# Kernel optimization log

Hardware: AMD Instinct MI355X
Metric: run time of the kernel (lower is better)

## Reference

```python
import jax, jax.numpy as jnp
import numpy as np

DIM = 1024
H = 16
D = DIM // H
CS = 64  # chunk_size
SCALE = D ** -0.5


def setup_inputs() -> dict:
    key = jax.random.key(0)
    k1, k2, k3 = jax.random.split(key, 3)
    B, N = 4, 4096
    x = jax.random.normal(k1, (B, N, DIM), dtype=jnp.float32)
    # torch nn.Linear(dim, 3*dim, bias=False): y = x @ W.T, W:[3*dim, dim].
    # We store the transposed layout W_qkv:[dim, 3*dim] so y = x @ W_qkv.
    W_qkv = jax.random.normal(k2, (DIM, 3 * DIM), dtype=jnp.float32) * (DIM ** -0.5)
    W_out = jax.random.normal(k3, (DIM, DIM), dtype=jnp.float32) * (DIM ** -0.5)
    return {"x": x, "W_qkv": W_qkv, "W_out": W_out}


def reference(x, W_qkv, W_out):
    B, N, C = x.shape
    qkv = (x @ W_qkv).reshape(B, N, 3, H, D)
    qkv = jnp.transpose(qkv, (2, 0, 3, 1, 4))  # [3,B,H,N,D]
    q, k, v = qkv[0], qkv[1], qkv[2]
    # N chosen divisible by CS, so no padding needed (pad=0 branch).
    nc = N // CS
    q = q.reshape(B, H, nc, CS, D)
    k = k.reshape(B, H, nc, CS, D)
    v = v.reshape(B, H, nc, CS, D)
    # Local quadratic attention within each chunk, causal mask.
    attn = jnp.einsum('bhcqd,bhckd->bhcqk', q, k) * SCALE
    mask = jnp.triu(jnp.ones((CS, CS), dtype=bool), k=1)
    attn = jnp.where(mask, jnp.float32(-65000.0), attn)
    attn = jax.nn.softmax(attn, axis=-1)
    out_local = jnp.einsum('bhcqk,bhckd->bhcqd', attn, v)
    # Cross-chunk linear term (num_chunks > 1): mean-pooled K/V, exclusive cumsum.
    chunk_k = k.mean(axis=3)  # [B,H,nc,D]
    chunk_v = v.mean(axis=3)
    cum_k = jnp.cumsum(chunk_k, axis=2)
    cum_v = jnp.cumsum(chunk_v, axis=2)
    zeros = jnp.zeros((B, H, 1, D), dtype=x.dtype)
    cum_k = jnp.concatenate([zeros, cum_k[:, :, :-1]], axis=2)
    cum_v = jnp.concatenate([zeros, cum_v[:, :, :-1]], axis=2)
    cross = jax.nn.sigmoid(jnp.einsum('bhcsd,bhcd->bhcs', q, cum_k) * SCALE)
    out = out_local + cross[..., None] * cum_v[:, :, :, None, :] * 0.5
    out = out.reshape(B, H, N, D)
    out = jnp.transpose(out, (0, 2, 1, 3)).reshape(B, N, C)
    return out @ W_out
```

## Files before the change

### kernel.cpp

```cpp
#include <hip/hip_runtime.h>
#include <stdint.h>

typedef __attribute__((ext_vector_type(4))) float f32x4;
typedef __attribute__((ext_vector_type(8))) short short8;
typedef unsigned short u16;

#define NH 16
#define HD 64
#define SEQ 4096
#define BATCH 4
#define NROWS (BATCH * SEQ)
#define DIMC 1024
#define QKVC 3072
#define SCALE 0.125f

__device__ __forceinline__ u16 f2bf(float f) {
  union { float f; uint32_t u; } v; v.f = f;
  uint32_t u = v.u;
  uint32_t r = (u + 0x7fffu + ((u >> 16) & 1u)) >> 16;
  return (u16)r;
}
__device__ __forceinline__ float bf2f(u16 h) {
  union { uint32_t u; float f; } v; v.u = ((uint32_t)h) << 16;
  return v.f;
}

__global__ __launch_bounds__(256) void cvt_kernel(const float* __restrict__ in,
                                                  u16* __restrict__ out, int n4) {
  int i = blockIdx.x * 256 + threadIdx.x;
  if (i >= n4) return;
  float4 v = ((const float4*)in)[i];
  ushort4 o;
  o.x = f2bf(v.x); o.y = f2bf(v.y); o.z = f2bf(v.z); o.w = f2bf(v.w);
  ((ushort4*)out)[i] = o;
}

__global__ __launch_bounds__(256) void transpose_cvt(const float* __restrict__ in,
                                                     u16* __restrict__ out, int R, int C) {
  __shared__ float t[32][33];
  int nbx = C >> 5;
  int bx = blockIdx.x % nbx, by = blockIdx.x / nbx;
  int r0 = by << 5, c0 = bx << 5;
  int tid = threadIdx.x;
#pragma unroll
  for (int i = 0; i < 4; i++) {
    int id = i * 256 + tid; int lr = id >> 5, lc = id & 31;
    t[lr][lc] = in[(size_t)(r0 + lr) * C + (c0 + lc)];
  }
  __syncthreads();
#pragma unroll
  for (int i = 0; i < 4; i++) {
    int id = i * 256 + tid; int lr = id >> 5, lc = id & 31;
    out[(size_t)(c0 + lr) * R + (r0 + lc)] = f2bf(t[lc][lr]);
  }
}

template <int OUT_BF16, int DO_SUMS>
__global__ __launch_bounds__(512, 2) void gemm_bt(const u16* __restrict__ A,
                                                  const u16* __restrict__ Bt,
                                                  void* __restrict__ Cv,
                                                  float* __restrict__ chk,
                                                  float* __restrict__ chv,
                                                  int M, int N, int K) {
  __shared__ __align__(16) u16 lds2[2][32768];
  int nbx = N >> 8;
  int nwg = gridDim.x;
  int bid = blockIdx.x;
  int cpx = nwg >> 3;
  int swz = (bid & 7) * cpx + (bid >> 3);
  int bx = swz % nbx, by = swz / nbx;
  int tid = threadIdx.x, lane = tid & 63, wv = tid >> 6;
  int wr = wv >> 2, wc = wv & 3;
  int lr = lane & 15, g = lane >> 4;
  int rx = lr & 7;
  int rsub = lane >> 3;
  int clog = (lane & 7) ^ rsub;

  const u16* Ap = A + (size_t)(by * 256) * K;
  const u16* Bp = Bt + (size_t)(bx * 256) * K;

  f32x4 acc[8][4];
#pragma unroll
  for (int m = 0; m < 8; m++)
#pragma unroll
    for (int n = 0; n < 4; n++) acc[m][n] = (f32x4){0.f, 0.f, 0.f, 0.f};

  short8 a0[4][2], a1[4][2], b0[2][2], b1[2][2];

#define ISSUE_A(HALF, L, T) do {                                                \
    int ru_ = (HALF) * 128 + (L) * 64 + wv * 8;                                 \
    const u16* g_ = Ap + (size_t)(ru_ + rsub) * K + (T) * 64 + clog * 8;        \
    __builtin_amdgcn_global_load_lds(                                           \
        (const __attribute__((address_space(1))) uint32_t*)g_,                  \
        (__attribute__((address_space(3))) uint32_t*)&lds2[(T) & 1][ru_ * 64],  \
        16, 0, 0);                                                              \
  } while (0)

#define ISSUE_B(HALF, L, T) do {                                                \
    int ru_ = (HALF) * 128 + (L) * 64 + wv * 8;                                 \
    const u16* g_ = Bp + (size_t)(ru_ + rsub) * K + (T) * 64 + clog * 8;        \
    __builtin_amdgcn_global_load_lds(                                           \
        (const __attribute__((address_space(1))) uint32_t*)g_,                  \
        (__attribute__((address_space(3)))                                      \
             uint32_t*)&lds2[(T) & 1][16384 + ru_ * 64],                        \
        16, 0, 0);                                                              \
  } while (0)

#define LDA4(DST, MH, T) do {                                                   \
    _Pragma("unroll")                                                           \
    for (int m2 = 0; m2 < 4; m2++) {                                            \
      int row_ = wr * 128 + ((MH) * 4 + m2) * 16 + lr;                          \
      const u16* bp_ = &lds2[(T) & 1][row_ * 64];                               \
      _Pragma("unroll")                                                         \
      for (int s = 0; s < 2; s++)                                               \
        DST[m2][s] = *(const short8*)(bp_ + (((s * 4 + g) ^ rx) << 3));         \
    }                                                                           \
  } while (0)

#define LDB(DST, NHh, T) do {                                                   \
    _Pragma("unroll")                                                           \
    for (int n2 = 0; n2 < 2; n2++) {                                            \
      int row_ = wc * 64 + ((NHh) * 2 + n2) * 16 + lr;                          \
      const u16* bp_ = &lds2[(T) & 1][16384 + row_ * 64];                       \
      _Pragma("unroll")                                                         \
      for (int s = 0; s < 2; s++)                                               \
        DST[n2][s] = *(const short8*)(bp_ + (((s * 4 + g) ^ rx) << 3));         \
    }                                                                           \
  } while (0)

#define MFMA_Q(MH, NHh, AA, BB) do {                                            \
    _Pragma("unroll")                                                           \
    for (int s = 0; s < 2; s++)                                                 \
      _Pragma("unroll")                                                         \
      for (int m2 = 0; m2 < 4; m2++)                                            \
        _Pragma("unroll")                                                       \
        for (int n2 = 0; n2 < 2; n2++)                                          \
          acc[(MH) * 4 + m2][(NHh) * 2 + n2] =                                  \
              __builtin_amdgcn_mfma_f32_16x16x32_bf16(                          \
                  AA[m2][s], BB[n2][s], acc[(MH) * 4 + m2][(NHh) * 2 + n2],     \
                  0, 0, 0);                                                     \
  } while (0)

  int NT = K >> 6;
  ISSUE_A(0, 0, 0); ISSUE_A(0, 1, 0); ISSUE_A(1, 0, 0); ISSUE_A(1, 1, 0);
  ISSUE_B(0, 0, 0); ISSUE_B(0, 1, 0); ISSUE_B(1, 0, 0); ISSUE_B(1, 1, 0);
  __syncthreads();

  for (int t = 0; t < NT; t++) {
    LDA4(a0, 0, t);
    LDB(b0, 0, t);
    __builtin_amdgcn_sched_barrier(0);
    if (t + 1 < NT) {
      ISSUE_A(0, 0, t + 1); ISSUE_A(0, 1, t + 1);
      ISSUE_A(1, 0, t + 1); ISSUE_A(1, 1, t + 1);
    }
    __builtin_amdgcn_sched_barrier(0);
    LDB(b1, 1, t);
    LDA4(a1, 1, t);
    __builtin_amdgcn_sched_barrier(0);
    if (t + 1 < NT) {
      ISSUE_B(0, 0, t + 1); ISSUE_B(0, 1, t + 1);
      ISSUE_B(1, 0, t + 1); ISSUE_B(1, 1, t + 1);
    }
    __builtin_amdgcn_sched_barrier(0);
    __builtin_amdgcn_s_setprio(1);
    MFMA_Q(0, 0, a0, b0);
    __builtin_amdgcn_sched_barrier(0);
    MFMA_Q(0, 1, a0, b1);
    __builtin_amdgcn_sched_barrier(0);
    MFMA_Q(1, 1, a1, b1);
    __builtin_amdgcn_sched_barrier(0);
    MFMA_Q(1, 0, a1, b0);
    __builtin_amdgcn_s_setprio(0);
    __syncthreads();
  }

#undef ISSUE_A
#undef ISSUE_B
#undef LDA4
#undef LDB
#undef MFMA_Q

  int rb = by * 256 + wr * 128, cb = bx * 256 + wc * 64;

  if (DO_SUMS && cb >= 1024) {
#pragma unroll
    for (int mh = 0; mh < 2; mh++)
#pragma unroll
      for (int n = 0; n < 4; n++) {
        float sum = 0.f;
#pragma unroll
        for (int m = mh * 4; m < mh * 4 + 4; m++)
#pragma unroll
          for (int r = 0; r < 4; r++) sum += acc[m][n][r];
        sum += __shfl_xor(sum, 16);
        sum += __shfl_xor(sum, 32);
        if (g == 0) {
          int grb = rb + mh * 64;
          int b = grb >> 12, c = (grb >> 6) & 63;
          int cg = cb + n * 16 + lr;
          int col = cg & 1023;
          int h = col >> 6, d = col & 63;
          float* dst = (cg < 2048) ? chk : chv;
          dst[(((size_t)(b * 16 + h)) * 64 + c) * 64 + d] = sum * 0.015625f;
        }
      }
  }

#pragma unroll
  for (int m = 0; m < 8; m++)
#pragma unroll
    for (int n = 0; n < 4; n++)
#pragma unroll
      for (int r = 0; r < 4; r++) {
        int rg = rb + m * 16 + g * 4 + r;
        int cg = cb + n * 16 + lr;
        float v = acc[m][n][r];
        if (OUT_BF16)
          ((u16*)Cv)[(size_t)rg * N + cg] = f2bf(v);
        else
          ((float*)Cv)[(size_t)rg * N + cg] = v;
      }
}

__global__ __launch_bounds__(256) void cumsum_excl(const float* __restrict__ ck,
                                                   const float* __restrict__ cv,
                                                   float* __restrict__ cuk,
                                                   float* __restrict__ cuv) {
  __shared__ float qk[4][64], qv[4][64];
  int bh = blockIdx.x;
  int d = threadIdx.x & 63, q = threadIdx.x >> 6;
  size_t base = ((size_t)bh * 64) * 64 + d;
  float sk = 0.f, sv = 0.f;
  for (int c = q * 16; c < q * 16 + 16; c++) {
    sk += ck[base + (size_t)c * 64];
    sv += cv[base + (size_t)c * 64];
  }
  qk[q][d] = sk; qv[q][d] = sv;
  __syncthreads();
  float ak = 0.f, av = 0.f;
  for (int p = 0; p < q; p++) { ak += qk[p][d]; av += qv[p][d]; }
  for (int c = q * 16; c < q * 16 + 16; c++) {
    size_t i = base + (size_t)c * 64;
    cuk[i] = ak; cuv[i] = av;
    ak += ck[i]; av += cv[i];
  }
}

__global__ __launch_bounds__(256) void attn_kernel(const u16* __restrict__ qkv,
                                                   const float* __restrict__ cuk,
                                                   const float* __restrict__ cuv,
                                                   u16* __restrict__ out) {
  int blk = blockIdx.x;
  int c = blk & 63, h = (blk >> 6) & 15, b = blk >> 10;
  int row0 = b * SEQ + c * 64;
  __shared__ u16 qp_s[64][88];
  __shared__ u16 k_s[64][88];
  __shared__ u16 vt_s[64][88];
  __shared__ u16 ck_s[64];
  __shared__ float cv_s[64];
  int tid = threadIdx.x;
  {
    if (tid < 64) {
      ck_s[tid] = f2bf(cuk[(size_t)blk * 64 + tid]);
      cv_s[tid] = cuv[(size_t)blk * 64 + tid];
    }
    int r = tid >> 2, qt = tid & 3;
    const u16* rp = qkv + (size_t)(row0 + r) * QKVC + h * 64 + qt * 16;
    uint4 q0 = *(const uint4*)rp;          uint4 q1 = *(const uint4*)(rp + 8);
    uint4 k0 = *(const uint4*)(rp + 1024); uint4 k1 = *(const uint4*)(rp + 1032);
    uint4 v0 = *(const uint4*)(rp + 2048); uint4 v1 = *(const uint4*)(rp + 2056);
    *(uint4*)&qp_s[r][qt * 16] = q0;    *(uint4*)&qp_s[r][qt * 16 + 8] = q1;
    *(uint4*)&k_s[r][qt * 16] = k0;     *(uint4*)&k_s[r][qt * 16 + 8] = k1;
    const u16* vv0 = (const u16*)&v0;   const u16* vv1 = (const u16*)&v1;
    int vcol = (r & 7) | ((((r >> 3) ^ qt) & 7) << 3);
#pragma unroll
    for (int j = 0; j < 8; j++) vt_s[qt * 16 + j][vcol] = vv0[j];
#pragma unroll
    for (int j = 0; j < 8; j++) vt_s[qt * 16 + 8 + j][vcol] = vv1[j];
  }
  __syncthreads();

  int lane = tid & 63, w = tid >> 6;
  int lr = lane & 15, g = lane >> 4;
  f32x4 accS[4];
#pragma unroll
  for (int n = 0; n < 4; n++) accS[n] = (f32x4){0.f, 0.f, 0.f, 0.f};
  f32x4 accC = (f32x4){0.f, 0.f, 0.f, 0.f};
  short8 zf = (short8){0, 0, 0, 0, 0, 0, 0, 0};
#pragma unroll
  for (int kt = 0; kt < 2; kt++) {
    int lk = kt * 32 + g * 8;
    short8 af = *(const short8*)&qp_s[w * 16 + lr][lk];
    short8 cf = (lr == 0) ? *(const short8*)&ck_s[lk] : zf;
    accC = __builtin_amdgcn_mfma_f32_16x16x32_bf16(af, cf, accC, 0, 0, 0);
#pragma unroll
    for (int n = 0; n < 4; n++) {
      short8 bf = *(const short8*)&k_s[n * 16 + lr][lk];
      accS[n] = __builtin_amdgcn_mfma_f32_16x16x32_bf16(af, bf, accS[n], 0, 0, 0);
    }
  }
  float crossv[4];
#pragma unroll
  for (int r4 = 0; r4 < 4; r4++) {
    int row = w * 16 + g * 4 + r4;
    float x[4];
    float mx = -3.4e38f;
#pragma unroll
    for (int n = 0; n < 4; n++) {
      int col = n * 16 + lr;
      x[n] = ((col & 63) > (row & 63)) ? -65000.0f : accS[n][r4] * SCALE;
      mx = fmaxf(mx, x[n]);
    }
    mx = fmaxf(mx, __shfl_xor(mx, 1));
    mx = fmaxf(mx, __shfl_xor(mx, 2));
    mx = fmaxf(mx, __shfl_xor(mx, 4));
    mx = fmaxf(mx, __shfl_xor(mx, 8));
    float p[4], sum = 0.f;
#pragma unroll
    for (int n = 0; n < 4; n++) { p[n] = __expf(x[n] - mx); sum += p[n]; }
    sum += __shfl_xor(sum, 1);
    sum += __shfl_xor(sum, 2);
    sum += __shfl_xor(sum, 4);
    sum += __shfl_xor(sum, 8);
    float inv = 1.0f / sum;
#pragma unroll
    for (int n = 0; n < 4; n++) qp_s[row][n * 16 + lr] = f2bf(p[n] * inv);
    float sg = 1.0f / (1.0f + __expf(-accC[r4] * SCALE));
    crossv[r4] = __shfl(sg, (lane & 48));
  }
  __syncthreads();
  f32x4 accO[4];
#pragma unroll
  for (int n = 0; n < 4; n++) accO[n] = (f32x4){0.f, 0.f, 0.f, 0.f};
#pragma unroll
  for (int kt = 0; kt < 2; kt++) {
    int lk = kt * 32 + g * 8;
    short8 pf = *(const short8*)&qp_s[w * 16 + lr][lk];
#pragma unroll
    for (int n = 0; n < 4; n++) {
      short8 vf = *(const short8*)&vt_s[n * 16 + lr][kt * 32 + ((g ^ n) << 3)];
      accO[n] = __builtin_amdgcn_mfma_f32_16x16x32_bf16(pf, vf, accO[n], 0, 0, 0);
    }
  }
#pragma unroll
  for (int n = 0; n < 4; n++)
#pragma unroll
    for (int r4 = 0; r4 < 4; r4++) {
      int row = w * 16 + g * 4 + r4;
      int col = n * 16 + lr;
      float v = accO[n][r4] + crossv[r4] * cv_s[col] * 0.5f;
      out[(size_t)(row0 + row) * DIMC + h * 64 + col] = f2bf(v);
    }
}

extern "C" void kernel_launch(void* const* d_in, const int* in_sizes, int n_in,
                              void* d_out, int out_size, void* d_ws, size_t ws_size,
                              hipStream_t stream) {
  const float* x = (const float*)d_in[0];
  const float* Wqkv = (const float*)d_in[1];
  const float* Wout = (const float*)d_in[2];
  char* ws = (char*)d_ws;
  size_t off = 0;
  auto alloc = [&](size_t b) {
    void* p = ws + off;
    off += (b + 255) & ~(size_t)255;
    return p;
  };
  u16* xb = (u16*)alloc((size_t)NROWS * DIMC * 2);
  u16* wqt = (u16*)alloc((size_t)QKVC * DIMC * 2);
  u16* wot = (u16*)alloc((size_t)DIMC * DIMC * 2);
  u16* qkvb = (u16*)alloc((size_t)NROWS * QKVC * 2);
  float* chk = (float*)alloc((size_t)4096 * 64 * 4);
  float* chv = (float*)alloc((size_t)4096 * 64 * 4);
  float* cuk = (float*)alloc((size_t)4096 * 64 * 4);
  float* cuv = (float*)alloc((size_t)4096 * 64 * 4);
  u16* attnb = xb;

  cvt_kernel<<<16384, 256, 0, stream>>>(x, xb, NROWS * DIMC / 4);
  transpose_cvt<<<3072, 256, 0, stream>>>(Wqkv, wqt, DIMC, QKVC);
  transpose_cvt<<<1024, 256, 0, stream>>>(Wout, wot, DIMC, DIMC);
  gemm_bt<1, 1><<<768, 512, 0, stream>>>(xb, wqt, qkvb, chk, chv, NROWS, QKVC, DIMC);
  cumsum_excl<<<64, 256, 0, stream>>>(chk, chv, cuk, cuv);
  attn_kernel<<<4096, 256, 0, stream>>>(qkvb, cuk, cuv, attnb);
  gemm_bt<0, 0><<<256, 512, 0, stream>>>(attnb, wot, d_out, nullptr, nullptr,
                                         NROWS, DIMC, DIMC);
}
```

Baseline: 196.6 us.

## Restructure bf16 GEMM main loop into 4-stage K=32 LDS pipeline

Replaces the double-buffered K=64 LDS tiles with a four-slot ring of K=32 tiles. Global-to-LDS loads are issued two stages ahead and gated by explicit vmcnt waits and s_barrier instead of __syncthreads. Register fragments are ping-ponged so LDS reads for the next stage overlap the current MFMAs, and the XOR swizzle is changed to match the narrower rows. The aim is to hide global load latency and reduce barrier stalls. The cost is more barriers per K, and the hand-written waitcnt logic is fragile.

```diff
diff --git a/kernel.cpp b/kernel.cpp
--- a/kernel.cpp
+++ b/kernel.cpp
@@ -62,7 +62,7 @@
                                                   float* __restrict__ chk,
                                                   float* __restrict__ chv,
                                                   int M, int N, int K) {
-  __shared__ __align__(16) u16 lds2[2][32768];
+  __shared__ __align__(16) u16 lds4[4][16384];
   int nbx = N >> 8;
   int nwg = gridDim.x;
   int bid = blockIdx.x;
@@ -72,9 +72,9 @@
   int tid = threadIdx.x, lane = tid & 63, wv = tid >> 6;
   int wr = wv >> 2, wc = wv & 3;
   int lr = lane & 15, g = lane >> 4;
-  int rx = lr & 7;
-  int rsub = lane >> 3;
-  int clog = (lane & 7) ^ rsub;
+  int rxk = (g ^ ((lr >> 1) & 3)) << 3;
+  int rsub4 = lane >> 2;
+  int clog = (lane & 3) ^ ((lane >> 3) & 3);
 
   const u16* Ap = A + (size_t)(by * 256) * K;
   const u16* Bp = Bt + (size_t)(bx * 256) * K;
@@ -85,101 +85,93 @@
 #pragma unroll
     for (int n = 0; n < 4; n++) acc[m][n] = (f32x4){0.f, 0.f, 0.f, 0.f};
 
-  short8 a0[4][2], a1[4][2], b0[2][2], b1[2][2];
-
-#define ISSUE_A(HALF, L, T) do {                                                \
-    int ru_ = (HALF) * 128 + (L) * 64 + wv * 8;                                 \
-    const u16* g_ = Ap + (size_t)(ru_ + rsub) * K + (T) * 64 + clog * 8;        \
+  short8 aA[8], bA[4], aB[8], bB[4];
+
+#define ISSUE_A(L, T) do {                                                      \
+    int ru_ = (L) * 128 + wv * 16;                                              \
+    const u16* g_ = Ap + (size_t)(ru_ + rsub4) * K + (T) * 32 + clog * 8;       \
     __builtin_amdgcn_global_load_lds(                                           \
         (const __attribute__((address_space(1))) uint32_t*)g_,                  \
-        (__attribute__((address_space(3))) uint32_t*)&lds2[(T) & 1][ru_ * 64],  \
+        (__attribute__((address_space(3))) uint32_t*)&lds4[(T) & 3][ru_ * 32],  \
         16, 0, 0);                                                              \
   } while (0)
 
-#define ISSUE_B(HALF, L, T) do {                                                \
-    int ru_ = (HALF) * 128 + (L) * 64 + wv * 8;                                 \
-    const u16* g_ = Bp + (size_t)(ru_ + rsub) * K + (T) * 64 + clog * 8;        \
+#define ISSUE_B(L, T) do {                                                      \
+    int ru_ = (L) * 128 + wv * 16;                                              \
+    const u16* g_ = Bp + (size_t)(ru_ + rsub4) * K + (T) * 32 + clog * 8;       \
     __builtin_amdgcn_global_load_lds(                                           \
         (const __attribute__((address_space(1))) uint32_t*)g_,                  \
         (__attribute__((address_space(3)))                                      \
-             uint32_t*)&lds2[(T) & 1][16384 + ru_ * 64],                        \
+             uint32_t*)&lds4[(T) & 3][8192 + ru_ * 32],                         \
         16, 0, 0);                                                              \
   } while (0)
 
-#define LDA4(DST, MH, T) do {                                                   \
+#define STAGE(T) do { ISSUE_A(0, T); ISSUE_A(1, T); ISSUE_B(0, T); ISSUE_B(1, T); } while (0)
+
+#define READS(SA, SB, T) do {                                                   \
+    const u16* ab_ = &lds4[(T) & 3][(wr * 128 + lr) * 32 + rxk];                \
+    const u16* bb_ = &lds4[(T) & 3][8192 + (wc * 64 + lr) * 32 + rxk];          \
     _Pragma("unroll")                                                           \
-    for (int m2 = 0; m2 < 4; m2++) {                                            \
-      int row_ = wr * 128 + ((MH) * 4 + m2) * 16 + lr;                          \
-      const u16* bp_ = &lds2[(T) & 1][row_ * 64];                               \
+    for (int m = 0; m < 8; m++) SA[m] = *(const short8*)(ab_ + m * 512);        \
+    _Pragma("unroll")                                                           \
+    for (int n = 0; n < 4; n++) SB[n] = *(const short8*)(bb_ + n * 512);        \
+  } while (0)
+
+#define MFMAS(SA, SB) do {                                                      \
+    _Pragma("unroll")                                                           \
+    for (int m = 0; m < 8; m++)                                                 \
       _Pragma("unroll")                                                         \
-      for (int s = 0; s < 2; s++)                                               \
-        DST[m2][s] = *(const short8*)(bp_ + (((s * 4 + g) ^ rx) << 3));         \
-    }                                                                           \
+      for (int n = 0; n < 4; n++)                                               \
+        acc[m][n] = __builtin_amdgcn_mfma_f32_16x16x32_bf16(                    \
+            SA[m], SB[n], acc[m][n], 0, 0, 0);                                  \
   } while (0)
 
-#define LDB(DST, NHh, T) do {                                                   \
-    _Pragma("unroll")                                                           \
-    for (int n2 = 0; n2 < 2; n2++) {                                            \
-      int row_ = wc * 64 + ((NHh) * 2 + n2) * 16 + lr;                          \
-      const u16* bp_ = &lds2[(T) & 1][16384 + row_ * 64];                       \
-      _Pragma("unroll")                                                         \
-      for (int s = 0; s < 2; s++)                                               \
-        DST[n2][s] = *(const short8*)(bp_ + (((s * 4 + g) ^ rx) << 3));         \
-    }                                                                           \
-  } while (0)
-
-#define MFMA_Q(MH, NHh, AA, BB) do {                                            \
-    _Pragma("unroll")                                                           \
-    for (int s = 0; s < 2; s++)                                                 \
-      _Pragma("unroll")                                                         \
-      for (int m2 = 0; m2 < 4; m2++)                                            \
-        _Pragma("unroll")                                                       \
-        for (int n2 = 0; n2 < 2; n2++)                                          \
-          acc[(MH) * 4 + m2][(NHh) * 2 + n2] =                                  \
-              __builtin_amdgcn_mfma_f32_16x16x32_bf16(                          \
-                  AA[m2][s], BB[n2][s], acc[(MH) * 4 + m2][(NHh) * 2 + n2],     \
-                  0, 0, 0);                                                     \
-  } while (0)
-
-  int NT = K >> 6;
-  ISSUE_A(0, 0, 0); ISSUE_A(0, 1, 0); ISSUE_A(1, 0, 0); ISSUE_A(1, 1, 0);
-  ISSUE_B(0, 0, 0); ISSUE_B(0, 1, 0); ISSUE_B(1, 0, 0); ISSUE_B(1, 1, 0);
-  __syncthreads();
-
-  for (int t = 0; t < NT; t++) {
-    LDA4(a0, 0, t);
-    LDB(b0, 0, t);
-    __builtin_amdgcn_sched_barrier(0);
-    if (t + 1 < NT) {
-      ISSUE_A(0, 0, t + 1); ISSUE_A(0, 1, t + 1);
-      ISSUE_A(1, 0, t + 1); ISSUE_A(1, 1, t + 1);
-    }
-    __builtin_amdgcn_sched_barrier(0);
-    LDB(b1, 1, t);
-    LDA4(a1, 1, t);
-    __builtin_amdgcn_sched_barrier(0);
-    if (t + 1 < NT) {
-      ISSUE_B(0, 0, t + 1); ISSUE_B(0, 1, t + 1);
-      ISSUE_B(1, 0, t + 1); ISSUE_B(1, 1, t + 1);
-    }
+  int NT = K >> 5;
+  STAGE(0); STAGE(1);
+  __builtin_amdgcn_sched_barrier(0);
+  asm volatile("s_waitcnt vmcnt(4)" ::: "memory");
+  __builtin_amdgcn_s_barrier();
+  READS(aA, bA, 0);
+  __builtin_amdgcn_sched_barrier(0);
+
+  for (int t = 0; t + 2 < NT; t += 2) {
+    STAGE(t + 2);
+    __builtin_amdgcn_sched_barrier(0);
+    asm volatile("s_waitcnt vmcnt(4)" ::: "memory");
+    __builtin_amdgcn_s_barrier();
+    READS(aB, bB, t + 1);
     __builtin_amdgcn_sched_barrier(0);
     __builtin_amdgcn_s_setprio(1);
-    MFMA_Q(0, 0, a0, b0);
-    __builtin_amdgcn_sched_barrier(0);
-    MFMA_Q(0, 1, a0, b1);
-    __builtin_amdgcn_sched_barrier(0);
-    MFMA_Q(1, 1, a1, b1);
-    __builtin_amdgcn_sched_barrier(0);
-    MFMA_Q(1, 0, a1, b0);
+    MFMAS(aA, bA);
     __builtin_amdgcn_s_setprio(0);
-    __syncthreads();
-  }
+    __builtin_amdgcn_sched_barrier(0);
+    if (t + 3 < NT) STAGE(t + 3);
+    __builtin_amdgcn_sched_barrier(0);
+    if (t + 3 < NT) asm volatile("s_waitcnt vmcnt(4)" ::: "memory");
+    else            asm volatile("s_waitcnt vmcnt(0)" ::: "memory");
+    __builtin_amdgcn_s_barrier();
+    READS(aA, bA, t + 2);
+    __builtin_amdgcn_sched_barrier(0);
+    __builtin_amdgcn_s_setprio(1);
+    MFMAS(aB, bB);
+    __builtin_amdgcn_s_setprio(0);
+    __builtin_amdgcn_sched_barrier(0);
+  }
+  asm volatile("s_waitcnt vmcnt(0)" ::: "memory");
+  __builtin_amdgcn_s_barrier();
+  READS(aB, bB, NT - 1);
+  __builtin_amdgcn_sched_barrier(0);
+  __builtin_amdgcn_s_setprio(1);
+  MFMAS(aA, bA);
+  __builtin_amdgcn_sched_barrier(0);
+  MFMAS(aB, bB);
+  __builtin_amdgcn_s_setprio(0);
 
 #undef ISSUE_A
 #undef ISSUE_B
-#undef LDA4
-#undef LDB
-#undef MFMA_Q
+#undef STAGE
+#undef READS
+#undef MFMAS
 
   int rb = by * 256 + wr * 128, cb = bx * 256 + wc * 64;
 
```

New measurement: 205.8 us. 4.7% more time.
